# Performance work log

Hardware: AMD Instinct MI355X
Metric: run time of the kernel (lower is better)

## Reference

```python
import jax, jax.numpy as jnp
import numpy as np

T = 1024
V = 512
K_BINS = jnp.array([1, 2, 3, 4, 5, 6, 7, 8, 12, 16, 24, 32, 48, 64, 96, 128], dtype=jnp.int32)
SPLIT_T = T // 2                      # int(T * 0.5)
CW = max(4, T // 20)                  # crossfade width = 51
FADE_START = SPLIT_T - CW // 2        # 487
FADE_END = SPLIT_T + CW // 2          # 537


def _early_weight():
    t = jnp.arange(T, dtype=jnp.float32)
    fade = 1.0 - (t - FADE_START) / (FADE_END - FADE_START)
    ew = jnp.where(t < FADE_START, 1.0, jnp.where(t < FADE_END, fade, 0.0))
    return ew.reshape(1, T, 1)


def setup_inputs() -> dict:
    key = jax.random.key(0)
    k = jax.random.split(key, 5)
    B = 64
    return {
        "x": jax.random.normal(k[0], (B, T, V), dtype=jnp.float32),
        "g_early_real": jax.random.normal(k[1], (V, 16), dtype=jnp.float32) * 0.1,
        "g_early_imag": jax.random.normal(k[2], (V, 16), dtype=jnp.float32) * 0.1,
        "g_late_real": jax.random.normal(k[3], (V, 16), dtype=jnp.float32) * 0.1,
        "g_late_imag": jax.random.normal(k[4], (V, 16), dtype=jnp.float32) * 0.1,
    }


def reference(x, g_early_real, g_early_imag, g_late_real, g_late_imag):
    # x: [B, T, V] real. rfft along time.
    X = jnp.fft.rfft(x, n=T, axis=1)              # [B, F, V] complex, F = T//2+1
    xb = X[:, K_BINS, :]                          # [B, K, V]
    # complex gain (1 + gr + i*gi), broadcast [1, K, V]
    g_e = (g_early_real + 1j * g_early_imag).T[None, :, :]
    g_l = (g_late_real + 1j * g_late_imag).T[None, :, :]
    Y_e = X.at[:, K_BINS, :].set(xb * (1.0 + g_e))
    Y_l = X.at[:, K_BINS, :].set(xb * (1.0 + g_l))
    y_early = jnp.fft.irfft(Y_e, n=T, axis=1)     # [B, T, V]
    y_late = jnp.fft.irfft(Y_l, n=T, axis=1)
    ew = _early_weight()
    return ew * y_early + (1.0 - ew) * y_late
```

## Files before the change

### kernel.cpp

```cpp
#include <hip/hip_runtime.h>
#include <math.h>

#define T_LEN 1024
#define VV 512
#define VVh 256
#define BB 64
#define NB 16
#define ANG_STEP 0.006135923151542565f
#define FADE_S 487
#define FADE_E 537
#define ATL 64

__device__ constexpr int KB[NB] = {1,2,3,4,5,6,7,8,12,16,24,32,48,64,96,128};

template<int TLEN>
__global__ __launch_bounds__(256, 2) void k_dft_partial(const float* __restrict__ x,
                                                        float* __restrict__ xpart,
                                                        int tc_count) {
    const int b   = blockIdx.x;
    const int tc  = blockIdx.y;
    const int tid = threadIdx.x;
    const int t0  = tc * TLEN;

    __shared__ float2 tab[TLEN][NB];
    for (int i = tid; i < TLEN * NB; i += 256) {
        int t = i >> 4, j = i & 15;
        int idx = (KB[j] * (t0 + t)) & (T_LEN - 1);
        float ss, cc; sincosf(ANG_STEP * (float)idx, &ss, &cc);
        tab[t][j] = make_float2(cc, ss);
    }
    __syncthreads();

    float xr0[NB], xi0[NB], xr1[NB], xi1[NB];
#pragma unroll
    for (int j = 0; j < NB; ++j) { xr0[j] = xi0[j] = xr1[j] = xi1[j] = 0.0f; }

    const float2* xrd = (const float2*)(x + ((size_t)b * T_LEN + t0) * VV) + tid;

#define DFT_T(TT, AV)                                           \
    do {                                                        \
        _Pragma("unroll")                                       \
        for (int j = 0; j < NB; ++j) {                          \
            float2 cs = tab[(TT)][j];                           \
            xr0[j] = fmaf((AV).x, cs.x, xr0[j]);                \
            xi0[j] = fmaf(-(AV).x, cs.y, xi0[j]);               \
            xr1[j] = fmaf((AV).y, cs.x, xr1[j]);                \
            xi1[j] = fmaf(-(AV).y, cs.y, xi1[j]);               \
        }                                                       \
    } while (0)

    float2 a0 = xrd[(size_t)0 * VVh];
    float2 a1 = xrd[(size_t)1 * VVh];
    float2 a2 = xrd[(size_t)2 * VVh];
    float2 a3 = xrd[(size_t)3 * VVh];
#pragma unroll 1
    for (int t = 0; t < TLEN - 4; t += 4) {
        float2 b0 = xrd[(size_t)(t + 4) * VVh];
        float2 b1 = xrd[(size_t)(t + 5) * VVh];
        float2 b2 = xrd[(size_t)(t + 6) * VVh];
        float2 b3 = xrd[(size_t)(t + 7) * VVh];
        DFT_T(t + 0, a0); DFT_T(t + 1, a1); DFT_T(t + 2, a2); DFT_T(t + 3, a3);
        a0 = b0; a1 = b1; a2 = b2; a3 = b3;
    }
    {
        const int t = TLEN - 4;
        DFT_T(t + 0, a0); DFT_T(t + 1, a1); DFT_T(t + 2, a2); DFT_T(t + 3, a3);
    }
#undef DFT_T

    float2* o = (float2*)(xpart + (size_t)(b * tc_count + tc) * 32 * VV) + tid;
#pragma unroll
    for (int j = 0; j < NB; ++j) {
        o[(size_t)j        * VVh] = make_float2(xr0[j], xr1[j]);
        o[(size_t)(NB + j) * VVh] = make_float2(xi0[j], xi1[j]);
    }
}

__global__ __launch_bounds__(256) void k_combine(const float* __restrict__ xpart,
                                                 const float* __restrict__ ger,
                                                 const float* __restrict__ gei,
                                                 const float* __restrict__ glr,
                                                 const float* __restrict__ gli,
                                                 float* __restrict__ H, int tc_count) {
    const int b   = blockIdx.x;
    const int j   = blockIdx.y;
    const int tid = threadIdx.x;
    const int v0  = tid * 2;

    float re0 = 0.f, re1 = 0.f, im0 = 0.f, im1 = 0.f;
#pragma unroll 8
    for (int tc = 0; tc < tc_count; ++tc) {
        const float2* p = (const float2*)(xpart + (size_t)(b * tc_count + tc) * 32 * VV) + tid;
        float2 a  = p[(size_t)j        * VVh];
        float2 bb = p[(size_t)(NB + j) * VVh];
        re0 += a.x;  re1 += a.y;
        im0 += bb.x; im1 += bb.y;
    }

    const float scale = 2.0f / (float)T_LEN;
    float er0 = ger[v0 * NB + j],       ei0 = gei[v0 * NB + j];
    float lr0 = glr[v0 * NB + j],       li0 = gli[v0 * NB + j];
    float er1 = ger[(v0 + 1) * NB + j], ei1 = gei[(v0 + 1) * NB + j];
    float lr1 = glr[(v0 + 1) * NB + j], li1 = gli[(v0 + 1) * NB + j];

    float here0 = (re0 * er0 - im0 * ei0) * scale;
    float heim0 = (re0 * ei0 + im0 * er0) * scale;
    float hlre0 = (re0 * lr0 - im0 * li0) * scale;
    float hlim0 = (re0 * li0 + im0 * lr0) * scale;
    float here1 = (re1 * er1 - im1 * ei1) * scale;
    float heim1 = (re1 * ei1 + im1 * er1) * scale;
    float hlre1 = (re1 * lr1 - im1 * li1) * scale;
    float hlim1 = (re1 * li1 + im1 * lr1) * scale;

    float2* o = (float2*)(H + (size_t)b * 64 * VV) + tid;
    o[(size_t)j        * VVh] = make_float2(here0, here1);
    o[(size_t)(16 + j) * VVh] = make_float2(-heim0, -heim1);
    o[(size_t)(32 + j) * VVh] = make_float2(hlre0, hlre1);
    o[(size_t)(48 + j) * VVh] = make_float2(-hlim0, -hlim1);
}

__global__ __launch_bounds__(256, 2) void k_apply_pure(const float* __restrict__ x,
                                                       const float* __restrict__ H,
                                                       float* __restrict__ out) {
    const int b    = blockIdx.x;
    const int ti   = blockIdx.y;
    const int tid  = threadIdx.x;
    const int tile = (ti < 7) ? ti : ti + 2;
    const int t0   = tile * ATL;
    const int qo   = (ti < 7) ? 0 : 32;

    __shared__ float2 tab[ATL][NB];
    for (int i = tid; i < ATL * NB; i += 256) {
        int t = i >> 4, j = i & 15;
        int idx = (KB[j] * (t0 + t)) & (T_LEN - 1);
        float ss, cc; sincosf(ANG_STEP * (float)idx, &ss, &cc);
        tab[t][j] = make_float2(cc, ss);
    }

    float hr0[NB], hi0[NB], hr1[NB], hi1[NB];
    const float2* hp = (const float2*)(H + (size_t)b * 64 * VV) + tid;
#pragma unroll
    for (int j = 0; j < NB; ++j) {
        float2 a  = hp[(size_t)(qo + j)      * VVh]; hr0[j] = a.x;  hr1[j] = a.y;
        float2 bq = hp[(size_t)(qo + 16 + j) * VVh]; hi0[j] = bq.x; hi1[j] = bq.y;
    }
    __syncthreads();

    const float2* xrd = (const float2*)(x + ((size_t)b * T_LEN + t0) * VV) + tid;
    float2*       ow  = (float2*)(out + ((size_t)b * T_LEN + t0) * VV) + tid;

#define APPLY_T(TT, AV)                                         \
    do {                                                        \
        float s0 = 0.f, s1 = 0.f;                               \
        _Pragma("unroll")                                       \
        for (int j = 0; j < NB; ++j) {                          \
            float2 cs = tab[(TT)][j];                           \
            s0 = fmaf(hr0[j], cs.x, s0);                        \
            s0 = fmaf(hi0[j], cs.y, s0);                        \
            s1 = fmaf(hr1[j], cs.x, s1);                        \
            s1 = fmaf(hi1[j], cs.y, s1);                        \
        }                                                       \
        ow[(size_t)(TT) * VVh] =                                \
            make_float2((AV).x + s0, (AV).y + s1);              \
    } while (0)

    float2 a0 = xrd[(size_t)0 * VVh];
    float2 a1 = xrd[(size_t)1 * VVh];
    float2 a2 = xrd[(size_t)2 * VVh];
    float2 a3 = xrd[(size_t)3 * VVh];
#pragma unroll 1
    for (int t = 0; t < ATL - 4; t += 4) {
        float2 b0 = xrd[(size_t)(t + 4) * VVh];
        float2 b1 = xrd[(size_t)(t + 5) * VVh];
        float2 b2 = xrd[(size_t)(t + 6) * VVh];
        float2 b3 = xrd[(size_t)(t + 7) * VVh];
        APPLY_T(t + 0, a0); APPLY_T(t + 1, a1); APPLY_T(t + 2, a2); APPLY_T(t + 3, a3);
        a0 = b0; a1 = b1; a2 = b2; a3 = b3;
    }
    {
        const int t = ATL - 4;
        APPLY_T(t + 0, a0); APPLY_T(t + 1, a1); APPLY_T(t + 2, a2); APPLY_T(t + 3, a3);
    }
#undef APPLY_T
}

__global__ __launch_bounds__(512) void k_apply_fade(const float* __restrict__ x,
                                                    const float* __restrict__ H,
                                                    float* __restrict__ out) {
    const int b   = blockIdx.x;
    const int tz  = blockIdx.y;
    const int tid = threadIdx.x;
    const int t0  = (7 + tz) * ATL;

    __shared__ float2 tab[ATL][NB];
    for (int i = tid; i < ATL * NB; i += 512) {
        int t = i >> 4, j = i & 15;
        int idx = (KB[j] * (t0 + t)) & (T_LEN - 1);
        float ss, cc; sincosf(ANG_STEP * (float)idx, &ss, &cc);
        tab[t][j] = make_float2(cc, ss);
    }

    float er[NB], ei[NB], lr[NB], li[NB];
    const float* hp = H + (size_t)b * 64 * VV + tid;
#pragma unroll
    for (int j = 0; j < NB; ++j) {
        er[j] = hp[(size_t)j        * VV];
        ei[j] = hp[(size_t)(16 + j) * VV];
        lr[j] = hp[(size_t)(32 + j) * VV];
        li[j] = hp[(size_t)(48 + j) * VV];
    }
    __syncthreads();

    const float* xrd = x + ((size_t)b * T_LEN + t0) * VV + tid;
    float*       ow  = out + ((size_t)b * T_LEN + t0) * VV + tid;

    for (int t = 0; t < ATL; t += 2) {
        float a0 = xrd[(size_t)(t + 0) * VV];
        float a1 = xrd[(size_t)(t + 1) * VV];
#pragma unroll
        for (int u = 0; u < 2; ++u) {
            float av = u ? a1 : a0;
            const int tg = t0 + t + u;
            float se = 0.f, sl = 0.f;
#pragma unroll
            for (int j = 0; j < NB; ++j) {
                float2 cs = tab[t + u][j];
                se = fmaf(er[j], cs.x, se); se = fmaf(ei[j], cs.y, se);
                sl = fmaf(lr[j], cs.x, sl); sl = fmaf(li[j], cs.y, sl);
            }
            float w = (tg < FADE_S) ? 1.0f
                    : ((tg < FADE_E) ? (1.0f - (float)(tg - FADE_S) * (1.0f / 50.0f)) : 0.0f);
            ow[(size_t)(t + u) * VV] = av + fmaf(w, se - sl, sl);
        }
    }
}

extern "C" void kernel_launch(void* const* d_in, const int* in_sizes, int n_in,
                              void* d_out, int out_size, void* d_ws, size_t ws_size,
                              hipStream_t stream) {
    (void)in_sizes; (void)n_in; (void)out_size;
    const float* x   = (const float*)d_in[0];
    const float* ger = (const float*)d_in[1];
    const float* gei = (const float*)d_in[2];
    const float* glr = (const float*)d_in[3];
    const float* gli = (const float*)d_in[4];
    float* out = (float*)d_out;

    const size_t hflts = (size_t)BB * 64 * VV;
    int TC;
    if (((size_t)BB * 8 * 32 * VV + hflts) * sizeof(float) <= ws_size)  TC = 8;
    else                                                                TC = 4;

    float* xpart = (float*)d_ws;
    float* H     = xpart + (size_t)BB * TC * 32 * VV;

    if (TC == 8) k_dft_partial<128><<<dim3(BB, 8), 256, 0, stream>>>(x, xpart, 8);
    else         k_dft_partial<256><<<dim3(BB, 4), 256, 0, stream>>>(x, xpart, 4);

    k_combine<<<dim3(BB, NB), 256, 0, stream>>>(xpart, ger, gei, glr, gli, H, TC);
    k_apply_pure<<<dim3(BB, 14), 256, 0, stream>>>(x, H, out);
    k_apply_fade<<<dim3(BB, 2),  512, 0, stream>>>(x, H, out);
}
```

Baseline: 133.1 us.

## Apply uniformly over all tiles, fix up only crossfade rows; deepen prefetch unroll

The apply kernel now covers every time tile, using early weights below the midpoint and late weights above. A small fixup kernel then recomputes only the 50 crossfade rows instead of two full 64-row tiles with double sums. Both the DFT and apply loops now prefetch 8 rows ahead instead of 4, and output stores are nontemporal. The cost is some rows written twice, plus a short dependent kernel tail.

```diff
diff --git a/kernel.cpp b/kernel.cpp
--- a/kernel.cpp
+++ b/kernel.cpp
@@ -10,6 +10,8 @@
 #define FADE_S 487
 #define FADE_E 537
 #define ATL 64
+
+typedef float v2f __attribute__((ext_vector_type(2)));
 
 __device__ constexpr int KB[NB] = {1,2,3,4,5,6,7,8,12,16,24,32,48,64,96,128};
 
@@ -53,18 +55,29 @@
     float2 a1 = xrd[(size_t)1 * VVh];
     float2 a2 = xrd[(size_t)2 * VVh];
     float2 a3 = xrd[(size_t)3 * VVh];
+    float2 a4 = xrd[(size_t)4 * VVh];
+    float2 a5 = xrd[(size_t)5 * VVh];
+    float2 a6 = xrd[(size_t)6 * VVh];
+    float2 a7 = xrd[(size_t)7 * VVh];
 #pragma unroll 1
-    for (int t = 0; t < TLEN - 4; t += 4) {
-        float2 b0 = xrd[(size_t)(t + 4) * VVh];
-        float2 b1 = xrd[(size_t)(t + 5) * VVh];
-        float2 b2 = xrd[(size_t)(t + 6) * VVh];
-        float2 b3 = xrd[(size_t)(t + 7) * VVh];
+    for (int t = 0; t < TLEN - 8; t += 8) {
+        float2 b0 = xrd[(size_t)(t +  8) * VVh];
+        float2 b1 = xrd[(size_t)(t +  9) * VVh];
+        float2 b2 = xrd[(size_t)(t + 10) * VVh];
+        float2 b3 = xrd[(size_t)(t + 11) * VVh];
+        float2 b4 = xrd[(size_t)(t + 12) * VVh];
+        float2 b5 = xrd[(size_t)(t + 13) * VVh];
+        float2 b6 = xrd[(size_t)(t + 14) * VVh];
+        float2 b7 = xrd[(size_t)(t + 15) * VVh];
         DFT_T(t + 0, a0); DFT_T(t + 1, a1); DFT_T(t + 2, a2); DFT_T(t + 3, a3);
+        DFT_T(t + 4, a4); DFT_T(t + 5, a5); DFT_T(t + 6, a6); DFT_T(t + 7, a7);
         a0 = b0; a1 = b1; a2 = b2; a3 = b3;
+        a4 = b4; a5 = b5; a6 = b6; a7 = b7;
     }
     {
-        const int t = TLEN - 4;
+        const int t = TLEN - 8;
         DFT_T(t + 0, a0); DFT_T(t + 1, a1); DFT_T(t + 2, a2); DFT_T(t + 3, a3);
+        DFT_T(t + 4, a4); DFT_T(t + 5, a5); DFT_T(t + 6, a6); DFT_T(t + 7, a7);
     }
 #undef DFT_T
 
@@ -119,15 +132,14 @@
     o[(size_t)(48 + j) * VVh] = make_float2(-hlim0, -hlim1);
 }
 
-__global__ __launch_bounds__(256, 2) void k_apply_pure(const float* __restrict__ x,
-                                                       const float* __restrict__ H,
-                                                       float* __restrict__ out) {
+__global__ __launch_bounds__(256, 2) void k_apply(const float* __restrict__ x,
+                                                  const float* __restrict__ H,
+                                                  float* __restrict__ out) {
     const int b    = blockIdx.x;
-    const int ti   = blockIdx.y;
+    const int tile = blockIdx.y;
     const int tid  = threadIdx.x;
-    const int tile = (ti < 7) ? ti : ti + 2;
     const int t0   = tile * ATL;
-    const int qo   = (ti < 7) ? 0 : 32;
+    const int qo   = (tile < 8) ? 0 : 32;
 
     __shared__ float2 tab[ATL][NB];
     for (int i = tid; i < ATL * NB; i += 256) {
@@ -147,7 +159,7 @@
     __syncthreads();
 
     const float2* xrd = (const float2*)(x + ((size_t)b * T_LEN + t0) * VV) + tid;
-    float2*       ow  = (float2*)(out + ((size_t)b * T_LEN + t0) * VV) + tid;
+    v2f*          ow  = (v2f*)(out + ((size_t)b * T_LEN + t0) * VV) + tid;
 
 #define APPLY_T(TT, AV)                                         \
     do {                                                        \
@@ -160,42 +172,56 @@
             s1 = fmaf(hr1[j], cs.x, s1);                        \
             s1 = fmaf(hi1[j], cs.y, s1);                        \
         }                                                       \
-        ow[(size_t)(TT) * VVh] =                                \
-            make_float2((AV).x + s0, (AV).y + s1);              \
+        v2f ov; ov.x = (AV).x + s0; ov.y = (AV).y + s1;         \
+        __builtin_nontemporal_store(ov,                         \
+            &ow[(size_t)(TT) * VVh]);                           \
     } while (0)
 
     float2 a0 = xrd[(size_t)0 * VVh];
     float2 a1 = xrd[(size_t)1 * VVh];
     float2 a2 = xrd[(size_t)2 * VVh];
     float2 a3 = xrd[(size_t)3 * VVh];
+    float2 a4 = xrd[(size_t)4 * VVh];
+    float2 a5 = xrd[(size_t)5 * VVh];
+    float2 a6 = xrd[(size_t)6 * VVh];
+    float2 a7 = xrd[(size_t)7 * VVh];
 #pragma unroll 1
-    for (int t = 0; t < ATL - 4; t += 4) {
-        float2 b0 = xrd[(size_t)(t + 4) * VVh];
-        float2 b1 = xrd[(size_t)(t + 5) * VVh];
-        float2 b2 = xrd[(size_t)(t + 6) * VVh];
-        float2 b3 = xrd[(size_t)(t + 7) * VVh];
+    for (int t = 0; t < ATL - 8; t += 8) {
+        float2 b0 = xrd[(size_t)(t +  8) * VVh];
+        float2 b1 = xrd[(size_t)(t +  9) * VVh];
+        float2 b2 = xrd[(size_t)(t + 10) * VVh];
+        float2 b3 = xrd[(size_t)(t + 11) * VVh];
+        float2 b4 = xrd[(size_t)(t + 12) * VVh];
+        float2 b5 = xrd[(size_t)(t + 13) * VVh];
+        float2 b6 = xrd[(size_t)(t + 14) * VVh];
+        float2 b7 = xrd[(size_t)(t + 15) * VVh];
         APPLY_T(t + 0, a0); APPLY_T(t + 1, a1); APPLY_T(t + 2, a2); APPLY_T(t + 3, a3);
+        APPLY_T(t + 4, a4); APPLY_T(t + 5, a5); APPLY_T(t + 6, a6); APPLY_T(t + 7, a7);
         a0 = b0; a1 = b1; a2 = b2; a3 = b3;
+        a4 = b4; a5 = b5; a6 = b6; a7 = b7;
     }
     {
-        const int t = ATL - 4;
+        const int t = ATL - 8;
         APPLY_T(t + 0, a0); APPLY_T(t + 1, a1); APPLY_T(t + 2, a2); APPLY_T(t + 3, a3);
+        APPLY_T(t + 4, a4); APPLY_T(t + 5, a5); APPLY_T(t + 6, a6); APPLY_T(t + 7, a7);
     }
 #undef APPLY_T
 }
 
-__global__ __launch_bounds__(512) void k_apply_fade(const float* __restrict__ x,
-                                                    const float* __restrict__ H,
-                                                    float* __restrict__ out) {
+__global__ __launch_bounds__(512) void k_fixup(const float* __restrict__ x,
+                                               const float* __restrict__ H,
+                                               float* __restrict__ out) {
     const int b   = blockIdx.x;
     const int tz  = blockIdx.y;
     const int tid = threadIdx.x;
-    const int t0  = (7 + tz) * ATL;
-
-    __shared__ float2 tab[ATL][NB];
-    for (int i = tid; i < ATL * NB; i += 512) {
+    const int ts  = tz ? 512 : FADE_S;
+    const int te  = tz ? FADE_E : 512;
+    const int nt  = te - ts;
+
+    __shared__ float2 tab[32][NB];
+    for (int i = tid; i < nt * NB; i += 512) {
         int t = i >> 4, j = i & 15;
-        int idx = (KB[j] * (t0 + t)) & (T_LEN - 1);
+        int idx = (KB[j] * (ts + t)) & (T_LEN - 1);
         float ss, cc; sincosf(ANG_STEP * (float)idx, &ss, &cc);
         tab[t][j] = make_float2(cc, ss);
     }
@@ -211,27 +237,21 @@
     }
     __syncthreads();
 
-    const float* xrd = x + ((size_t)b * T_LEN + t0) * VV + tid;
-    float*       ow  = out + ((size_t)b * T_LEN + t0) * VV + tid;
-
-    for (int t = 0; t < ATL; t += 2) {
-        float a0 = xrd[(size_t)(t + 0) * VV];
-        float a1 = xrd[(size_t)(t + 1) * VV];
-#pragma unroll
-        for (int u = 0; u < 2; ++u) {
-            float av = u ? a1 : a0;
-            const int tg = t0 + t + u;
-            float se = 0.f, sl = 0.f;
-#pragma unroll
-            for (int j = 0; j < NB; ++j) {
-                float2 cs = tab[t + u][j];
-                se = fmaf(er[j], cs.x, se); se = fmaf(ei[j], cs.y, se);
-                sl = fmaf(lr[j], cs.x, sl); sl = fmaf(li[j], cs.y, sl);
-            }
-            float w = (tg < FADE_S) ? 1.0f
-                    : ((tg < FADE_E) ? (1.0f - (float)(tg - FADE_S) * (1.0f / 50.0f)) : 0.0f);
-            ow[(size_t)(t + u) * VV] = av + fmaf(w, se - sl, sl);
+    const float* xrd = x + ((size_t)b * T_LEN + ts) * VV + tid;
+    float*       ow  = out + ((size_t)b * T_LEN + ts) * VV + tid;
+
+    for (int t = 0; t < nt; ++t) {
+        float av = xrd[(size_t)t * VV];
+        const int tg = ts + t;
+        float se = 0.f, sl = 0.f;
+#pragma unroll
+        for (int j = 0; j < NB; ++j) {
+            float2 cs = tab[t][j];
+            se = fmaf(er[j], cs.x, se); se = fmaf(ei[j], cs.y, se);
+            sl = fmaf(lr[j], cs.x, sl); sl = fmaf(li[j], cs.y, sl);
         }
+        float w = 1.0f - (float)(tg - FADE_S) * (1.0f / 50.0f);
+        ow[(size_t)t * VV] = av + fmaf(w, se - sl, sl);
     }
 }
 
@@ -258,6 +278,6 @@
     else         k_dft_partial<256><<<dim3(BB, 4), 256, 0, stream>>>(x, xpart, 4);
 
     k_combine<<<dim3(BB, NB), 256, 0, stream>>>(xpart, ger, gei, glr, gli, H, TC);
-    k_apply_pure<<<dim3(BB, 14), 256, 0, stream>>>(x, H, out);
-    k_apply_fade<<<dim3(BB, 2),  512, 0, stream>>>(x, H, out);
-}
+    k_apply<<<dim3(BB, 16), 256, 0, stream>>>(x, H, out);
+    k_fixup<<<dim3(BB, 2), 512, 0, stream>>>(x, H, out);
+}
```

Result: faster. 115.4 us (-13.3%).
